# Performance work log

Hardware: AMD Instinct MI355X
Metric: run time of the kernel (lower is better)

## Reference

```python
import jax, jax.numpy as jnp
import numpy as np
from jax import lax

NB, D_MODEL, D_INNER, D_STATE, K, L, BATCH, NCLS, DT_RANK = 3, 512, 1024, 8, 4, 2048, 4, 10, 32


def setup_inputs() -> dict:
    key = jax.random.key(0)
    ks = jax.random.split(key, 12)
    s = 0.02
    inp = {
        "x": jax.random.normal(ks[0], (BATCH, L, D_MODEL), jnp.float32),
        "in_proj_w": s * jax.random.normal(ks[1], (NB, D_MODEL, 2 * D_INNER), jnp.float32),
        "conv_w": s * jax.random.normal(ks[2], (NB, D_INNER, K), jnp.float32),
        "conv_b": jnp.zeros((NB, D_INNER), jnp.float32),
        "x_proj_w": s * jax.random.normal(ks[3], (NB, D_INNER, DT_RANK + 2 * D_STATE), jnp.float32),
        "dt_proj_w": s * jax.random.normal(ks[4], (NB, DT_RANK, D_INNER), jnp.float32),
        "dt_proj_b": jnp.full((NB, D_INNER), -4.0, jnp.float32),
        "A_log": jnp.broadcast_to(jnp.log(jnp.arange(1, D_STATE + 1, dtype=jnp.float32)), (NB, D_INNER, D_STATE)).copy(),
        "D": jnp.ones((NB, D_INNER), jnp.float32),
        "out_proj_w": s * jax.random.normal(ks[5], (NB, D_INNER, D_MODEL), jnp.float32),
        "cls_w": s * jax.random.normal(ks[6], (D_MODEL, NCLS), jnp.float32),
        "cls_b": jnp.zeros((NCLS,), jnp.float32),
    }
    return inp


def _mamba_block(x, Wi, cw, cb, Wx, Wdt, bdt, A_log, Dp, Wo):
    # x: [B, L, d_model]
    Bsz, Lx, _ = x.shape
    d_inner = Dp.shape[0]
    d_state = A_log.shape[-1]
    dt_rank = Wdt.shape[0]
    xz = x @ Wi                               # [B, L, 2*d_inner]
    u, z = jnp.split(xz, 2, axis=-1)
    # causal depthwise conv1d over time
    uc = jnp.swapaxes(u, 1, 2)                # [B, d_inner, L]
    k = cw.shape[-1]
    uc = lax.conv_general_dilated(uc, cw[:, None, :], window_strides=(1,),
                                  padding=[(k - 1, 0)], feature_group_count=d_inner,
                                  dimension_numbers=("NCH", "OIH", "NCH"))
    u = jax.nn.silu(jnp.swapaxes(uc, 1, 2) + cb)   # [B, L, d_inner]
    dbl = u @ Wx                                   # [B, L, dt_rank + 2*d_state]
    dt = dbl[..., :dt_rank]
    Bm = dbl[..., dt_rank:dt_rank + d_state]
    Cm = dbl[..., dt_rank + d_state:]
    delta = jax.nn.softplus(dt @ Wdt + bdt)        # [B, L, d_inner]
    A = -jnp.exp(A_log)                            # [d_inner, d_state]

    def step(h, inp):
        d_t, B_t, C_t, u_t = inp                   # [B,d],[B,n],[B,n],[B,d]
        h = jnp.exp(d_t[..., None] * A) * h + (d_t * u_t)[..., None] * B_t[:, None, :]
        return h, jnp.einsum("bdn,bn->bd", h, C_t)

    xs = (jnp.swapaxes(delta, 0, 1), jnp.swapaxes(Bm, 0, 1),
          jnp.swapaxes(Cm, 0, 1), jnp.swapaxes(u, 0, 1))
    h0 = jnp.zeros((Bsz, d_inner, d_state), x.dtype)
    _, ys = lax.scan(step, h0, xs)                 # ys: [L, B, d_inner]
    y = jnp.swapaxes(ys, 0, 1) + u * Dp
    y = y * jax.nn.silu(z)
    return x + y @ Wo                              # residual


def reference(x, in_proj_w, conv_w, conv_b, x_proj_w, dt_proj_w, dt_proj_b, A_log, D, out_proj_w, cls_w, cls_b):
    nb = in_proj_w.shape[0]
    for i in range(nb):
        x = _mamba_block(x, in_proj_w[i], conv_w[i], conv_b[i], x_proj_w[i],
                         dt_proj_w[i], dt_proj_b[i], A_log[i], D[i], out_proj_w[i])
    pooled = jnp.mean(x, axis=1)                   # AdaptiveAvgPool1d(1) over seq
    return pooled @ cls_w + cls_b                  # [B, num_classes]
```

## Files before the change

kernel.cpp:

```cpp
#include <hip/hip_runtime.h>
#include <cstddef>
#include <cstdint>

#define L_SEQ   2048
#define BATCH_N 4
#define DMODEL  512
#define DINNER  1024
#define DSTATE  8
#define KCONV   4
#define DTRANK  32
#define NBLK    3
#define NCLS_N  10
#define MROWS   (BATCH_N * L_SEQ)
#define DBLW    48
#define NSPLIT  8

#define LC2 16
#define NC2 (L_SEQ / LC2)
#define VD  2
#define SCAN_THREADS 512
#define SCAN_WAVES   (SCAN_THREADS / 64)

#define CGRP 8
#define CPG  (NC2 / CGRP)

typedef __attribute__((ext_vector_type(8))) short bf16x8;
typedef __attribute__((ext_vector_type(4))) short bf16x4;
typedef __attribute__((ext_vector_type(2))) short bf16x2;
typedef __attribute__((ext_vector_type(4))) float f32x4;

__device__ __forceinline__ float sigmoid_fast(float x) { return 1.f / (1.f + __expf(-x)); }
__device__ __forceinline__ float silu_fast(float x)    { return x * sigmoid_fast(x); }
__device__ __forceinline__ float softplus_fast(float x){
    return fmaxf(x, 0.f) + __logf(1.f + __expf(-fabsf(x)));
}
__device__ __forceinline__ float exp2_fast(float x) {
#if __has_builtin(__builtin_amdgcn_exp2f)
    return __builtin_amdgcn_exp2f(x);
#else
    return __expf(x * 0.69314718055994531f);
#endif
}
#define LOG2E 1.44269504088896341f

__device__ __forceinline__ unsigned short f2bf(float f) {
    union { float f; uint32_t u; } v; v.f = f;
    const uint32_t u = v.u;
    return (unsigned short)((u + 0x7fffu + ((u >> 16) & 1u)) >> 16);
}
__device__ __forceinline__ float bf2f(unsigned short h) {
    union { uint32_t u; float f; } v; v.u = ((uint32_t)h) << 16;
    return v.f;
}
__device__ __forceinline__ float bf2f_s(short h) { return bf2f((unsigned short)h); }

__device__ __forceinline__ void load_lds16(const void* g, void* l) {
    __builtin_amdgcn_global_load_lds(
        (const __attribute__((address_space(1))) unsigned int*)g,
        (__attribute__((address_space(3))) unsigned int*)l,
        16, 0, 0);
}

template <int K, int NT, int EPI>
__global__ __launch_bounds__(256) void gemm_bf16(
    const unsigned short* __restrict__ A, int lda,
    const unsigned short* __restrict__ Bt, int ldb,
    int ldc,
    unsigned short* __restrict__ Obf,
    float* __restrict__ pool)
{
    constexpr int BCH   = NT / 8;
    constexpr int NTW   = NT / 32;
    constexpr int STAGE = 8192 + NT * 64;
    constexpr int EPIL  = 128 * (NT + 8);
    constexpr int SMEM  = (STAGE > EPIL) ? STAGE : EPIL;
    __shared__ unsigned short sMem[SMEM];
    unsigned short* sA = sMem;
    unsigned short* sB = sMem + 8192;

    const int tid  = threadIdx.x;
    const int lane = tid & 63;
    const int wave = tid >> 6;
    const int m0 = blockIdx.y * 128;
    const int n0 = blockIdx.x * NT;
    const int wm = (wave >> 1) * 64;
    const int wn = (wave & 1) * (NT / 2);
    const int lm = lane & 15;
    const int lq = lane >> 4;

    const int srow = lane >> 3;
    const int scol = ((lane & 7) ^ srow) * 8;

    f32x4 acc[4][NTW];
    #pragma unroll
    for (int i = 0; i < 4; ++i)
        #pragma unroll
        for (int j = 0; j < NTW; ++j) acc[i][j] = (f32x4){0.f, 0.f, 0.f, 0.f};

    for (int k0 = 0; k0 < K; k0 += 64) {
        #pragma unroll
        for (int c = wave; c < 16; c += 4)
            load_lds16(A + (size_t)(m0 + c * 8 + srow) * lda + k0 + scol, &sA[c * 512]);
        #pragma unroll
        for (int c = wave; c < BCH; c += 4)
            load_lds16(Bt + (size_t)(n0 + c * 8 + srow) * ldb + k0 + scol, &sB[c * 512]);
        __syncthreads();
        #pragma unroll
        for (int ks = 0; ks < 2; ++ks) {
            bf16x8 aF[4], bF[NTW];
            #pragma unroll
            for (int mt = 0; mt < 4; ++mt) {
                const int row = wm + mt * 16 + lm;
                aF[mt] = *(const bf16x8*)&sA[row * 64 + (((ks * 4 + lq) ^ (lm & 7)) * 8)];
            }
            #pragma unroll
            for (int nt = 0; nt < NTW; ++nt) {
                const int row = wn + nt * 16 + lm;
                bF[nt] = *(const bf16x8*)&sB[row * 64 + (((ks * 4 + lq) ^ (lm & 7)) * 8)];
            }
            #pragma unroll
            for (int mt = 0; mt < 4; ++mt)
                #pragma unroll
                for (int nt = 0; nt < NTW; ++nt)
                    acc[mt][nt] = __builtin_amdgcn_mfma_f32_16x16x32_bf16(
                        aF[mt], bF[nt], acc[mt][nt], 0, 0, 0);
        }
        __syncthreads();
    }

    unsigned short* sOut = sMem;
    #pragma unroll
    for (int mt = 0; mt < 4; ++mt) {
        #pragma unroll
        for (int nt = 0; nt < NTW; ++nt) {
            #pragma unroll
            for (int r = 0; r < 4; ++r) {
                const int row = wm + mt * 16 + lq * 4 + r;
                const int col = wn + nt * 16 + lm;
                float v = acc[mt][nt][r];
                if (EPI >= 2) {
                    const size_t gi = (size_t)(m0 + row) * ldc + n0 + col;
                    v += bf2f(Obf[gi]);
                }
                sOut[row * (NT + 8) + col] = f2bf(v);
            }
        }
    }
    __syncthreads();
    #pragma unroll
    for (int j = 0; j < NT / 16; ++j) {
        const int idx = j * 256 + tid;
        const int row = idx / (NT / 8);
        const int cpos = (idx % (NT / 8)) * 8;
        *(bf16x8*)&Obf[(size_t)(m0 + row) * ldc + n0 + cpos] =
            *(const bf16x8*)&sOut[row * (NT + 8) + cpos];
    }
    if (EPI == 3) {
        const int b = m0 >> 11;
        const int col = tid & (NT - 1);
        const int q = tid / NT;
        constexpr int RPQ = 128 / (256 / NT);
        float s = 0.f;
        #pragma unroll
        for (int r = q * RPQ; r < (q + 1) * RPQ; ++r)
            s += bf2f(sOut[r * (NT + 8) + col]);
        atomicAdd(&pool[b * DMODEL + n0 + col], s);
    }
}

__global__ __launch_bounds__(256) void gemm_xproj(
    const unsigned short* __restrict__ ub,
    const unsigned short* __restrict__ Wxt,
    float* __restrict__ Xp)
{
    const int tid = threadIdx.x, lane = tid & 63, wave = tid >> 6;
    const int lm = lane & 15, lq = lane >> 4;
    const int rowA = blockIdx.x * 128 + wave * 32;
    const int split = blockIdx.y;
    const int k0 = split * (DINNER / NSPLIT);

    f32x4 acc[2][3];
    #pragma unroll
    for (int i = 0; i < 2; ++i)
        #pragma unroll
        for (int j = 0; j < 3; ++j) acc[i][j] = (f32x4){0.f, 0.f, 0.f, 0.f};

    #pragma unroll
    for (int kk = 0; kk < DINNER / NSPLIT; kk += 32) {
        const int k = k0 + kk;
        bf16x8 aF[2], bF[3];
        #pragma unroll
        for (int mt = 0; mt < 2; ++mt)
            aF[mt] = *(const bf16x8*)&ub[(size_t)(rowA + mt * 16 + lm) * DINNER + k + lq * 8];
        #pragma unroll
        for (int nt = 0; nt < 3; ++nt)
            bF[nt] = *(const bf16x8*)&Wxt[(size_t)(nt * 16 + lm) * DINNER + k + lq * 8];
        #pragma unroll
        for (int mt = 0; mt < 2; ++mt)
            #pragma unroll
            for (int nt = 0; nt < 3; ++nt)
                acc[mt][nt] = __builtin_amdgcn_mfma_f32_16x16x32_bf16(
                    aF[mt], bF[nt], acc[mt][nt], 0, 0, 0);
    }
    float* dst = Xp + (size_t)split * MROWS * DBLW;
    #pragma unroll
    for (int mt = 0; mt < 2; ++mt)
        #pragma unroll
        for (int nt = 0; nt < 3; ++nt)
            #pragma unroll
            for (int r = 0; r < 4; ++r)
                dst[(size_t)(rowA + mt * 16 + lq * 4 + r) * DBLW
                    + nt * 16 + lm] = acc[mt][nt][r];
}

__global__ __launch_bounds__(256) void transpose_cast(
    const float* __restrict__ in, unsigned short* __restrict__ out,
    int Kdim, int Ndim, size_t in_stride, size_t out_stride)
{
    __shared__ float s[32][33];
    const float* ip = in + blockIdx.z * in_stride;
    unsigned short* op = out + blockIdx.z * out_stride;
    const int bx = blockIdx.x * 32;
    const int by = blockIdx.y * 32;
    const int t = threadIdx.x;
    const int r = t >> 3;
    const int c4 = (t & 7) * 4;

    const int row = by + r;
    if (bx + c4 + 3 < Ndim) {
        float4 v = *(const float4*)&ip[(size_t)row * Ndim + bx + c4];
        s[r][c4 + 0] = v.x; s[r][c4 + 1] = v.y; s[r][c4 + 2] = v.z; s[r][c4 + 3] = v.w;
    } else {
        for (int i = 0; i < 4; ++i) {
            const int col = bx + c4 + i;
            s[r][c4 + i] = (col < Ndim) ? ip[(size_t)row * Ndim + col] : 0.f;
        }
    }
    __syncthreads();
    if (bx + r < Ndim) {
        unsigned short w0 = f2bf(s[c4 + 0][r]), w1 = f2bf(s[c4 + 1][r]);
        unsigned short w2 = f2bf(s[c4 + 2][r]), w3 = f2bf(s[c4 + 3][r]);
        uint2 pk;
        pk.x = (uint32_t)w0 | ((uint32_t)w1 << 16);
        pk.y = (uint32_t)w2 | ((uint32_t)w3 << 16);
        *(uint2*)&op[(size_t)(bx + r) * Kdim + by + c4] = pk;
    }
}

__global__ void cast_init(const float* __restrict__ in, unsigned short* __restrict__ outb,
                          float* __restrict__ pooled_accum, int n4) {
    const int i = blockIdx.x * 256 + threadIdx.x;
    if (i < BATCH_N * DMODEL / 4)
        ((f32x4*)pooled_accum)[i] = (f32x4){0.f, 0.f, 0.f, 0.f};
    if (i >= n4) return;
    float4 v = ((const float4*)in)[i];
    uint2 pk;
    pk.x = (uint32_t)f2bf(v.x) | ((uint32_t)f2bf(v.y) << 16);
    pk.y = (uint32_t)f2bf(v.z) | ((uint32_t)f2bf(v.w) << 16);
    ((uint2*)outb)[i] = pk;
}

__global__ void conv_w_transpose(const float* __restrict__ cw, float* __restrict__ cwt) {
    const int i = blockIdx.x * 256 + threadIdx.x;
    if (i >= NBLK * DINNER * KCONV) return;
    const int blk = i >> 12;
    const int rem = i & 4095;
    const int d = rem >> 2;
    const int k = rem & 3;
    cwt[blk * 4096 + k * DINNER + d] = cw[blk * 4096 + d * KCONV + k];
}

__global__ __launch_bounds__(256) void conv_silu_kernel(
    const unsigned short* __restrict__ xz,
    const float* __restrict__ cwt,
    const float* __restrict__ cb,
    unsigned short* __restrict__ ub)
{
    const int idx = blockIdx.x * 256 + threadIdx.x;
    const int dv = idx & 127;
    const int m  = idx >> 7;
    const int t  = m & (L_SEQ - 1);
    const int d0 = dv * 8;

    float acc[8];
    {
        float4 c0 = *(const float4*)&cb[d0];
        float4 c1 = *(const float4*)&cb[d0 + 4];
        acc[0] = c0.x; acc[1] = c0.y; acc[2] = c0.z; acc[3] = c0.w;
        acc[4] = c1.x; acc[5] = c1.y; acc[6] = c1.z; acc[7] = c1.w;
    }
    #pragma unroll
    for (int k = 0; k < KCONV; ++k) {
        const int tt = t + k - (KCONV - 1);
        if (tt >= 0) {
            bf16x8 xv = *(const bf16x8*)&xz[(size_t)(m - t + tt) * (2 * DINNER) + d0];
            float4 w0 = *(const float4*)&cwt[k * DINNER + d0];
            float4 w1 = *(const float4*)&cwt[k * DINNER + d0 + 4];
            acc[0] = fmaf(bf2f_s(xv[0]), w0.x, acc[0]);
            acc[1] = fmaf(bf2f_s(xv[1]), w0.y, acc[1]);
            acc[2] = fmaf(bf2f_s(xv[2]), w0.z, acc[2]);
            acc[3] = fmaf(bf2f_s(xv[3]), w0.w, acc[3]);
            acc[4] = fmaf(bf2f_s(xv[4]), w1.x, acc[4]);
            acc[5] = fmaf(bf2f_s(xv[5]), w1.y, acc[5]);
            acc[6] = fmaf(bf2f_s(xv[6]), w1.z, acc[6]);
            acc[7] = fmaf(bf2f_s(xv[7]), w1.w, acc[7]);
        }
    }
    bf16x8 o;
    #pragma unroll
    for (int j = 0; j < 8; ++j) o[j] = (short)f2bf(silu_fast(acc[j]));
    *(bf16x8*)&ub[(size_t)m * DINNER + d0] = o;
}

__device__ __forceinline__ void dt_recompute_lds(
    unsigned short* sDelta,
    const float* __restrict__ Xp,
    const unsigned short* __restrict__ Wdtt,
    const float* __restrict__ bdt,
    size_t m0, int lane, int wave)
{
    const int lm = lane & 15, lq = lane >> 4;
    float x[8] = {0.f, 0.f, 0.f, 0.f, 0.f, 0.f, 0.f, 0.f};
    #pragma unroll
    for (int sp = 0; sp < NSPLIT; ++sp) {
        const float* p = &Xp[((size_t)sp * MROWS + m0 + lm) * DBLW + lq * 8];
        float4 x0 = *(const float4*)p;
        float4 x1 = *(const float4*)(p + 4);
        x[0] += x0.x; x[1] += x0.y; x[2] += x0.z; x[3] += x0.w;
        x[4] += x1.x; x[5] += x1.y; x[6] += x1.z; x[7] += x1.w;
    }
    bf16x8 aF;
    #pragma unroll
    for (int j = 0; j < 8; ++j) aF[j] = (short)f2bf(x[j]);

    constexpr int NPW = DINNER / (16 * SCAN_WAVES);
    #pragma unroll
    for (int nt = 0; nt < NPW; ++nt) {
        const int col16 = wave * (DINNER / SCAN_WAVES) + nt * 16;
        bf16x8 bF = *(const bf16x8*)&Wdtt[(size_t)(col16 + lm) * DTRANK + lq * 8];
        f32x4 acc = (f32x4){0.f, 0.f, 0.f, 0.f};
        acc = __builtin_amdgcn_mfma_f32_16x16x32_bf16(aF, bF, acc, 0, 0, 0);
        const float bias = bdt[col16 + lm];
        #pragma unroll
        for (int r = 0; r < 4; ++r)
            sDelta[(lq * 4 + r) * DINNER + col16 + lm] =
                f2bf(softplus_fast(acc[r] + bias));
    }
}

__global__ __launch_bounds__(SCAN_THREADS) void scan_chunk_kernel(
    const unsigned short* __restrict__ ub,
    const float* __restrict__ Xp,
    const unsigned short* __restrict__ Wdtt,
    const float* __restrict__ bdt,
    const float* __restrict__ A_log,
    float* __restrict__ PSbuf)
{
    const int c = blockIdx.x;
    const int b = blockIdx.y;
    const int tid = threadIdx.x;
    const int lane = tid & 63;
    const int wave = tid >> 6;
    const int d0 = tid * VD;

    __shared__ unsigned short sDelta[LC2 * DINNER];
    __shared__ float sB[LC2][DSTATE];

    const size_t m0 = (size_t)b * L_SEQ + c * LC2;

    dt_recompute_lds(sDelta, Xp, Wdtt, bdt, m0, lane, wave);
    if (tid < LC2 * DSTATE) {
        const int r = tid >> 3, n = tid & 7;
        float s = 0.f;
        #pragma unroll
        for (int sp = 0; sp < NSPLIT; ++sp)
            s += Xp[((size_t)sp * MROWS + m0 + r) * DBLW + DTRANK + n];
        sB[r][n] = s;
    }
    __syncthreads();

    float a[DSTATE * VD], S[DSTATE * VD];
    float dtsum[VD];
    #pragma unroll
    for (int v = 0; v < VD; ++v) dtsum[v] = 0.f;
    #pragma unroll
    for (int n = 0; n < DSTATE; ++n)
        #pragma unroll
        for (int v = 0; v < VD; ++v) {
            a[n * VD + v] = -__expf(A_log[(d0 + v) * DSTATE + n]) * LOG2E;
            S[n * VD + v] = 0.f;
        }

    for (int r = 0; r < LC2; ++r) {
        const size_t m = m0 + r;
        bf16x2 dv = *(const bf16x2*)&sDelta[r * DINNER + d0];
        bf16x2 uv = *(const bf16x2*)&ub[m * DINNER + d0];
        float dt[VD], du[VD];
        #pragma unroll
        for (int v = 0; v < VD; ++v) {
            dt[v] = bf2f_s(dv[v]);
            du[v] = dt[v] * bf2f_s(uv[v]);
            dtsum[v] += dt[v];
        }
        #pragma unroll
        for (int n = 0; n < DSTATE; ++n) {
            const float bn = sB[r][n];
            #pragma unroll
            for (int v = 0; v < VD; ++v) {
                const float e = exp2_fast(dt[v] * a[n * VD + v]);
                S[n * VD + v] = fmaf(e, S[n * VD + v], du[v] * bn);
            }
        }
    }

    const size_t nb = (size_t)(b * NC2 + c) * DSTATE;
    #pragma unroll
    for (int n = 0; n < DSTATE; ++n) {
        const float P0 = exp2_fast(a[n * VD + 0] * dtsum[0]);
        const float P1 = exp2_fast(a[n * VD + 1] * dtsum[1]);
        float* dst = &PSbuf[(nb + n) * (DINNER * 2) + (size_t)d0 * 2];
        *(f32x4*)dst = (f32x4){P0, S[n * VD + 0], P1, S[n * VD + 1]};
    }
}

__global__ __launch_bounds__(512) void scan_combine_kernel(
    const float* __restrict__ PSbuf,
    float* __restrict__ Hbuf)
{
    const int dl = threadIdx.x & 63;
    const int g  = threadIdx.x >> 6;
    const int d  = blockIdx.x * 64 + dl;
    const int n  = blockIdx.y;
    const int b  = blockIdx.z;

    __shared__ float sP[CGRP][64];
    __shared__ float sS[CGRP][64];

    const int c0 = g * CPG;
    float Pseg = 1.f, Sseg = 0.f;
    #pragma unroll 4
    for (int cc = 0; cc < CPG; ++cc) {
        const size_t row = (size_t)(b * NC2 + c0 + cc) * DSTATE + n;
        const float2 ps = *(const float2*)&PSbuf[row * (DINNER * 2) + (size_t)d * 2];
        Pseg *= ps.x;
        Sseg = fmaf(ps.x, Sseg, ps.y);
    }
    sP[g][dl] = Pseg;
    sS[g][dl] = Sseg;
    __syncthreads();

    float h = 0.f;
    for (int gg = 0; gg < g; ++gg)
        h = fmaf(sP[gg][dl], h, sS[gg][dl]);

    #pragma unroll 4
    for (int cc = 0; cc < CPG; ++cc) {
        const size_t row = (size_t)(b * NC2 + c0 + cc) * DSTATE + n;
        const float2 ps = *(const float2*)&PSbuf[row * (DINNER * 2) + (size_t)d * 2];
        Hbuf[row * DINNER + d] = h;
        h = fmaf(ps.x, h, ps.y);
    }
}

__global__ __launch_bounds__(SCAN_THREADS) void scan_out_kernel(
    const unsigned short* __restrict__ ub,
    const float* __restrict__ Xp,
    const unsigned short* __restrict__ Wdtt,
    const float* __restrict__ bdt,
    const unsigned short* __restrict__ xz,
    const float* __restrict__ A_log,
    const float* __restrict__ Dp,
    const float* __restrict__ Hin,
    unsigned short* __restrict__ ybuf)
{
    const int c = blockIdx.x;
    const int b = blockIdx.y;
    const int tid = threadIdx.x;
    const int lane = tid & 63;
    const int wave = tid >> 6;
    const int d0 = tid * VD;

    __shared__ unsigned short sDelta[LC2 * DINNER];
    __shared__ float sB[LC2][DSTATE];
    __shared__ float sC[LC2][DSTATE];

    const size_t m0 = (size_t)b * L_SEQ + c * LC2;

    dt_recompute_lds(sDelta, Xp, Wdtt, bdt, m0, lane, wave);
    if (tid < LC2 * 2 * DSTATE) {
        const int r = tid >> 4, j = tid & 15;
        float s = 0.f;
        #pragma unroll
        for (int sp = 0; sp < NSPLIT; ++sp)
            s += Xp[((size_t)sp * MROWS + m0 + r) * DBLW + DTRANK + j];
        if (j < DSTATE) sB[r][j] = s;
        else            sC[r][j - DSTATE] = s;
    }
    __syncthreads();

    float a[DSTATE * VD], h[DSTATE * VD];
    const size_t base = ((size_t)(b * NC2 + c) * DSTATE) * DINNER + d0;
    #pragma unroll
    for (int n = 0; n < DSTATE; ++n) {
        float2 hv = *(const float2*)&Hin[base + (size_t)n * DINNER];
        h[n * VD + 0] = hv.x; h[n * VD + 1] = hv.y;
        #pragma unroll
        for (int v = 0; v < VD; ++v)
            a[n * VD + v] = -__expf(A_log[(d0 + v) * DSTATE + n]) * LOG2E;
    }
    float Dd[VD];
    {
        float2 dv2 = *(const float2*)&Dp[d0];
        Dd[0] = dv2.x; Dd[1] = dv2.y;
    }

    for (int r = 0; r < LC2; ++r) {
        const size_t m = m0 + r;
        bf16x2 dv = *(const bf16x2*)&sDelta[r * DINNER + d0];
        bf16x2 uv = *(const bf16x2*)&ub[m * DINNER + d0];
        bf16x2 zv = *(const bf16x2*)&xz[m * (2 * DINNER) + DINNER + d0];
        float dt[VD], ut[VD], du[VD], acc[VD];
        #pragma unroll
        for (int v = 0; v < VD; ++v) {
            dt[v] = bf2f_s(dv[v]);
            ut[v] = bf2f_s(uv[v]);
            du[v] = dt[v] * ut[v];
            acc[v] = 0.f;
        }
        #pragma unroll
        for (int n = 0; n < DSTATE; ++n) {
            const float bn = sB[r][n];
            const float cn = sC[r][n];
            #pragma unroll
            for (int v = 0; v < VD; ++v) {
                const float e = exp2_fast(dt[v] * a[n * VD + v]);
                h[n * VD + v] = fmaf(e, h[n * VD + v], du[v] * bn);
                acc[v] = fmaf(h[n * VD + v], cn, acc[v]);
            }
        }
        bf16x2 o;
        #pragma unroll
        for (int v = 0; v < VD; ++v)
            o[v] = (short)f2bf(fmaf(ut[v], Dd[v], acc[v]) * silu_fast(bf2f_s(zv[v])));
        *(bf16x2*)&ybuf[m * DINNER + d0] = o;
    }
}

__global__ __launch_bounds__(512) void pool_cls_kernel(
    const float* __restrict__ pooled_accum,
    const float* __restrict__ w,
    const float* __restrict__ bias,
    float* __restrict__ out)
{
    __shared__ float sp[DMODEL];
    const int b = blockIdx.x;
    const int dm = threadIdx.x;
    sp[dm] = pooled_accum[b * DMODEL + dm] * (1.f / (float)L_SEQ);
    __syncthreads();
    if (dm < NCLS_N) {
        float acc = bias[dm];
        for (int k = 0; k < DMODEL; ++k)
            acc = fmaf(sp[k], w[k * NCLS_N + dm], acc);
        out[b * NCLS_N + dm] = acc;
    }
}

extern "C" void kernel_launch(void* const* d_in, const int* in_sizes, int n_in,
                              void* d_out, int out_size, void* d_ws, size_t ws_size,
                              hipStream_t stream) {
    const float* x_in      = (const float*)d_in[0];
    const float* in_proj_w = (const float*)d_in[1];
    const float* conv_w    = (const float*)d_in[2];
    const float* conv_b    = (const float*)d_in[3];
    const float* x_proj_w  = (const float*)d_in[4];
    const float* dt_proj_w = (const float*)d_in[5];
    const float* dt_proj_b = (const float*)d_in[6];
    const float* A_log     = (const float*)d_in[7];
    const float* Dp        = (const float*)d_in[8];
    const float* out_proj_w= (const float*)d_in[9];
    const float* cls_w     = (const float*)d_in[10];
    const float* cls_b     = (const float*)d_in[11];
    float* out = (float*)d_out;

    char* w = (char*)d_ws;
    auto alloc = [&](size_t bytes) { char* p = w; w += (bytes + 255) & ~(size_t)255; return p; };
    unsigned short* xz_bf  = (unsigned short*)alloc((size_t)MROWS * 2 * DINNER * 2);
    unsigned short* ub     = (unsigned short*)alloc((size_t)MROWS * DINNER * 2);
    float*          Xp     = (float*)         alloc((size_t)NSPLIT * MROWS * DBLW * 4);
    float*          PSbuf  = (float*)         alloc((size_t)BATCH_N * NC2 * DSTATE * DINNER * 2 * 4);
    float*          Hbuf   = (float*)         alloc((size_t)BATCH_N * NC2 * DSTATE * DINNER * 4);
    unsigned short* xb     = (unsigned short*)alloc((size_t)MROWS * DMODEL * 2);
    unsigned short* ybuf   = (unsigned short*)alloc((size_t)MROWS * DINNER * 2);
    unsigned short* Wit    = (unsigned short*)alloc((size_t)NBLK * 2048 * 512 * 2);
    unsigned short* Wot    = (unsigned short*)alloc((size_t)NBLK * 512 * 1024 * 2);
    unsigned short* Wxt    = (unsigned short*)alloc((size_t)NBLK * DBLW * 1024 * 2);
    unsigned short* Wdtt   = (unsigned short*)alloc((size_t)NBLK * 1024 * DTRANK * 2);
    float*          cwt    = (float*)         alloc((size_t)NBLK * KCONV * DINNER * 4);
    float*          pooled = (float*)         alloc((size_t)BATCH_N * DMODEL * 4);

    cast_init<<<(MROWS * DMODEL / 4) / 256, 256, 0, stream>>>(
        x_in, xb, pooled, MROWS * DMODEL / 4);
    transpose_cast<<<dim3(2048 / 32, 512 / 32, NBLK), 256, 0, stream>>>(
        in_proj_w, Wit, 512, 2048, (size_t)512 * 2048, (size_t)2048 * 512);
    transpose_cast<<<dim3(512 / 32, 1024 / 32, NBLK), 256, 0, stream>>>(
        out_proj_w, Wot, 1024, 512, (size_t)1024 * 512, (size_t)512 * 1024);
    transpose_cast<<<dim3(2, 1024 / 32, NBLK), 256, 0, stream>>>(
        x_proj_w, Wxt, 1024, DBLW, (size_t)1024 * DBLW, (size_t)DBLW * 1024);
    transpose_cast<<<dim3(1024 / 32, 1, NBLK), 256, 0, stream>>>(
        dt_proj_w, Wdtt, DTRANK, 1024, (size_t)DTRANK * 1024, (size_t)1024 * DTRANK);
    conv_w_transpose<<<(NBLK * DINNER * KCONV + 255) / 256, 256, 0, stream>>>(conv_w, cwt);

    for (int blk = 0; blk < NBLK; ++blk) {
        const unsigned short* Wit_b  = Wit  + (size_t)blk * 2048 * 512;
        const unsigned short* Wot_b  = Wot  + (size_t)blk * 512 * 1024;
        const unsigned short* Wxt_b  = Wxt  + (size_t)blk * DBLW * 1024;
        const unsigned short* Wdtt_b = Wdtt + (size_t)blk * 1024 * DTRANK;
        const float* cwt_b = cwt + (size_t)blk * KCONV * DINNER;
        const float* cb  = conv_b    + (size_t)blk * DINNER;
        const float* bdt = dt_proj_b + (size_t)blk * DINNER;
        const float* Al  = A_log     + (size_t)blk * DINNER * DSTATE;
        const float* Dv  = Dp        + (size_t)blk * DINNER;

        gemm_bf16<512, 128, 0><<<dim3(2048 / 128, MROWS / 128), 256, 0, stream>>>(
            xb, DMODEL, Wit_b, DMODEL, 2 * DINNER, xz_bf, nullptr);
        conv_silu_kernel<<<(MROWS * 128) / 256, 256, 0, stream>>>(
            xz_bf, cwt_b, cb, ub);
        gemm_xproj<<<dim3(MROWS / 128, NSPLIT), 256, 0, stream>>>(ub, Wxt_b, Xp);
        {
            dim3 gridA(NC2, BATCH_N);
            scan_chunk_kernel<<<gridA, SCAN_THREADS, 0, stream>>>(
                ub, Xp, Wdtt_b, bdt, Al, PSbuf);
            scan_combine_kernel<<<dim3(DINNER / 64, DSTATE, BATCH_N), 512, 0, stream>>>(
                PSbuf, Hbuf);
            scan_out_kernel<<<gridA, SCAN_THREADS, 0, stream>>>(
                ub, Xp, Wdtt_b, bdt, xz_bf, Al, Dv, Hbuf, ybuf);
        }
        if (blk < NBLK - 1)
            gemm_bf16<1024, 64, 2><<<dim3(DMODEL / 64, MROWS / 128), 256, 0, stream>>>(
                ybuf, DINNER, Wot_b, DINNER, DMODEL, xb, nullptr);
        else
            gemm_bf16<1024, 64, 3><<<dim3(DMODEL / 64, MROWS / 128), 256, 0, stream>>>(
                ybuf, DINNER, Wot_b, DINNER, DMODEL, xb, pooled);
    }

    pool_cls_kernel<<<BATCH_N, DMODEL, 0, stream>>>(pooled, cls_w, cls_b, out);
}
```

Baseline: 551.1 us.

## Split scan blocks over d_inner halves and pre-reduce x_proj partials

The scan chunk and scan output kernels now handle half of d_inner per block, one channel per thread, which doubles the grid to give more parallelism and lower register pressure. A new xp_reduce kernel sums the split-K x_proj partials once, so the scan kernels no longer each re-read all eight splits. A prep kernel computes -exp(A_log)*log2e once, removing that per-block transcendental work. The cost is an extra launch and buffer, narrower (scalar bf16) global loads, and the dt projection recomputed in twice as many blocks.

```diff
diff --git a/kernel.cpp b/kernel.cpp
--- a/kernel.cpp
+++ b/kernel.cpp
@@ -17,7 +17,7 @@
 
 #define LC2 16
 #define NC2 (L_SEQ / LC2)
-#define VD  2
+#define DHALF (DINNER / 2)
 #define SCAN_THREADS 512
 #define SCAN_WAVES   (SCAN_THREADS / 64)
 
@@ -213,6 +213,23 @@
                     + nt * 16 + lm] = acc[mt][nt][r];
 }
 
+__global__ __launch_bounds__(256) void xp_reduce(
+    const float* __restrict__ Xp, float* __restrict__ dblsum)
+{
+    const int i = blockIdx.x * 256 + threadIdx.x;
+    f32x4 s = (f32x4){0.f, 0.f, 0.f, 0.f};
+    #pragma unroll
+    for (int sp = 0; sp < NSPLIT; ++sp)
+        s += ((const f32x4*)(Xp + (size_t)sp * MROWS * DBLW))[i];
+    ((f32x4*)dblsum)[i] = s;
+}
+
+__global__ void prep_negA(const float* __restrict__ A_log, float* __restrict__ negA) {
+    const int i = blockIdx.x * 256 + threadIdx.x;
+    if (i < NBLK * DINNER * DSTATE)
+        negA[i] = -__expf(A_log[i]) * LOG2E;
+}
+
 __global__ __launch_bounds__(256) void transpose_cast(
     const float* __restrict__ in, unsigned short* __restrict__ out,
     int Kdim, int Ndim, size_t in_stride, size_t out_stride)
@@ -314,112 +331,97 @@
 
 __device__ __forceinline__ void dt_recompute_lds(
     unsigned short* sDelta,
-    const float* __restrict__ Xp,
+    const float* __restrict__ dblsum,
     const unsigned short* __restrict__ Wdtt,
     const float* __restrict__ bdt,
-    size_t m0, int lane, int wave)
+    size_t m0, int lane, int wave, int dbase)
 {
     const int lm = lane & 15, lq = lane >> 4;
-    float x[8] = {0.f, 0.f, 0.f, 0.f, 0.f, 0.f, 0.f, 0.f};
-    #pragma unroll
-    for (int sp = 0; sp < NSPLIT; ++sp) {
-        const float* p = &Xp[((size_t)sp * MROWS + m0 + lm) * DBLW + lq * 8];
+    bf16x8 aF;
+    {
+        const float* p = &dblsum[(m0 + lm) * DBLW + lq * 8];
         float4 x0 = *(const float4*)p;
         float4 x1 = *(const float4*)(p + 4);
-        x[0] += x0.x; x[1] += x0.y; x[2] += x0.z; x[3] += x0.w;
-        x[4] += x1.x; x[5] += x1.y; x[6] += x1.z; x[7] += x1.w;
-    }
-    bf16x8 aF;
-    #pragma unroll
-    for (int j = 0; j < 8; ++j) aF[j] = (short)f2bf(x[j]);
-
-    constexpr int NPW = DINNER / (16 * SCAN_WAVES);
+        aF[0] = (short)f2bf(x0.x); aF[1] = (short)f2bf(x0.y);
+        aF[2] = (short)f2bf(x0.z); aF[3] = (short)f2bf(x0.w);
+        aF[4] = (short)f2bf(x1.x); aF[5] = (short)f2bf(x1.y);
+        aF[6] = (short)f2bf(x1.z); aF[7] = (short)f2bf(x1.w);
+    }
+    constexpr int NPW = DHALF / (16 * SCAN_WAVES);
     #pragma unroll
     for (int nt = 0; nt < NPW; ++nt) {
-        const int col16 = wave * (DINNER / SCAN_WAVES) + nt * 16;
+        const int cloc = wave * (DHALF / SCAN_WAVES) + nt * 16;
+        const int col16 = dbase + cloc;
         bf16x8 bF = *(const bf16x8*)&Wdtt[(size_t)(col16 + lm) * DTRANK + lq * 8];
         f32x4 acc = (f32x4){0.f, 0.f, 0.f, 0.f};
         acc = __builtin_amdgcn_mfma_f32_16x16x32_bf16(aF, bF, acc, 0, 0, 0);
         const float bias = bdt[col16 + lm];
         #pragma unroll
         for (int r = 0; r < 4; ++r)
-            sDelta[(lq * 4 + r) * DINNER + col16 + lm] =
+            sDelta[(lq * 4 + r) * DHALF + cloc + lm] =
                 f2bf(softplus_fast(acc[r] + bias));
     }
 }
 
 __global__ __launch_bounds__(SCAN_THREADS) void scan_chunk_kernel(
     const unsigned short* __restrict__ ub,
-    const float* __restrict__ Xp,
+    const float* __restrict__ dblsum,
     const unsigned short* __restrict__ Wdtt,
     const float* __restrict__ bdt,
-    const float* __restrict__ A_log,
+    const float* __restrict__ negA,
     float* __restrict__ PSbuf)
 {
-    const int c = blockIdx.x;
-    const int b = blockIdx.y;
+    const int c  = blockIdx.x;
+    const int dh = blockIdx.y;
+    const int b  = blockIdx.z;
     const int tid = threadIdx.x;
     const int lane = tid & 63;
     const int wave = tid >> 6;
-    const int d0 = tid * VD;
-
-    __shared__ unsigned short sDelta[LC2 * DINNER];
+    const int dbase = dh * DHALF;
+    const int d = dbase + tid;
+
+    __shared__ unsigned short sDelta[LC2 * DHALF];
     __shared__ float sB[LC2][DSTATE];
 
     const size_t m0 = (size_t)b * L_SEQ + c * LC2;
 
-    dt_recompute_lds(sDelta, Xp, Wdtt, bdt, m0, lane, wave);
+    dt_recompute_lds(sDelta, dblsum, Wdtt, bdt, m0, lane, wave, dbase);
     if (tid < LC2 * DSTATE) {
         const int r = tid >> 3, n = tid & 7;
-        float s = 0.f;
-        #pragma unroll
-        for (int sp = 0; sp < NSPLIT; ++sp)
-            s += Xp[((size_t)sp * MROWS + m0 + r) * DBLW + DTRANK + n];
-        sB[r][n] = s;
+        sB[r][n] = dblsum[(m0 + r) * DBLW + DTRANK + n];
     }
     __syncthreads();
 
-    float a[DSTATE * VD], S[DSTATE * VD];
-    float dtsum[VD];
-    #pragma unroll
-    for (int v = 0; v < VD; ++v) dtsum[v] = 0.f;
-    #pragma unroll
-    for (int n = 0; n < DSTATE; ++n)
-        #pragma unroll
-        for (int v = 0; v < VD; ++v) {
-            a[n * VD + v] = -__expf(A_log[(d0 + v) * DSTATE + n]) * LOG2E;
-            S[n * VD + v] = 0.f;
-        }
+    float a[DSTATE], S[DSTATE];
+    {
+        float4 a0 = *(const float4*)&negA[(size_t)d * DSTATE];
+        float4 a1 = *(const float4*)&negA[(size_t)d * DSTATE + 4];
+        a[0] = a0.x; a[1] = a0.y; a[2] = a0.z; a[3] = a0.w;
+        a[4] = a1.x; a[5] = a1.y; a[6] = a1.z; a[7] = a1.w;
+    }
+    #pragma unroll
+    for (int n = 0; n < DSTATE; ++n) S[n] = 0.f;
+    float dtsum = 0.f;
 
     for (int r = 0; r < LC2; ++r) {
         const size_t m = m0 + r;
-        bf16x2 dv = *(const bf16x2*)&sDelta[r * DINNER + d0];
-        bf16x2 uv = *(const bf16x2*)&ub[m * DINNER + d0];
-        float dt[VD], du[VD];
-        #pragma unroll
-        for (int v = 0; v < VD; ++v) {
-            dt[v] = bf2f_s(dv[v]);
-            du[v] = dt[v] * bf2f_s(uv[v]);
-            dtsum[v] += dt[v];
+        const float dt = bf2f(sDelta[r * DHALF + tid]);
+        const float du = dt * bf2f(ub[m * DINNER + d]);
+        dtsum += dt;
+        #pragma unroll
+        for (int n = 0; n < DSTATE; ++n) {
+            const float e = exp2_fast(dt * a[n]);
+            S[n] = fmaf(e, S[n], du * sB[r][n]);
         }
-        #pragma unroll
-        for (int n = 0; n < DSTATE; ++n) {
-            const float bn = sB[r][n];
-            #pragma unroll
-            for (int v = 0; v < VD; ++v) {
-                const float e = exp2_fast(dt[v] * a[n * VD + v]);
-                S[n * VD + v] = fmaf(e, S[n * VD + v], du[v] * bn);
-            }
-        }
     }
 
     const size_t nb = (size_t)(b * NC2 + c) * DSTATE;
     #pragma unroll
     for (int n = 0; n < DSTATE; ++n) {
-        const float P0 = exp2_fast(a[n * VD + 0] * dtsum[0]);
-        const float P1 = exp2_fast(a[n * VD + 1] * dtsum[1]);
-        float* dst = &PSbuf[(nb + n) * (DINNER * 2) + (size_t)d0 * 2];
-        *(f32x4*)dst = (f32x4){P0, S[n * VD + 0], P1, S[n * VD + 1]};
+        float2 ps;
+        ps.x = exp2_fast(a[n] * dtsum);
+        ps.y = S[n];
+        *(float2*)&PSbuf[(nb + n) * (DINNER * 2) + (size_t)d * 2] = ps;
     }
 }
 
@@ -464,85 +466,66 @@
 
 __global__ __launch_bounds__(SCAN_THREADS) void scan_out_kernel(
     const unsigned short* __restrict__ ub,
-    const float* __restrict__ Xp,
+    const float* __restrict__ dblsum,
     const unsigned short* __restrict__ Wdtt,
     const float* __restrict__ bdt,
     const unsigned short* __restrict__ xz,
-    const float* __restrict__ A_log,
+    const float* __restrict__ negA,
     const float* __restrict__ Dp,
     const float* __restrict__ Hin,
     unsigned short* __restrict__ ybuf)
 {
-    const int c = blockIdx.x;
-    const int b = blockIdx.y;
+    const int c  = blockIdx.x;
+    const int dh = blockIdx.y;
+    const int b  = blockIdx.z;
     const int tid = threadIdx.x;
     const int lane = tid & 63;
     const int wave = tid >> 6;
-    const int d0 = tid * VD;
-
-    __shared__ unsigned short sDelta[LC2 * DINNER];
+    const int dbase = dh * DHALF;
+    const int d = dbase + tid;
+
+    __shared__ unsigned short sDelta[LC2 * DHALF];
     __shared__ float sB[LC2][DSTATE];
     __shared__ float sC[LC2][DSTATE];
 
     const size_t m0 = (size_t)b * L_SEQ + c * LC2;
 
-    dt_recompute_lds(sDelta, Xp, Wdtt, bdt, m0, lane, wave);
+    dt_recompute_lds(sDelta, dblsum, Wdtt, bdt, m0, lane, wave, dbase);
     if (tid < LC2 * 2 * DSTATE) {
         const int r = tid >> 4, j = tid & 15;
-        float s = 0.f;
-        #pragma unroll
-        for (int sp = 0; sp < NSPLIT; ++sp)
-            s += Xp[((size_t)sp * MROWS + m0 + r) * DBLW + DTRANK + j];
-        if (j < DSTATE) sB[r][j] = s;
-        else            sC[r][j - DSTATE] = s;
+        const float v = dblsum[(m0 + r) * DBLW + DTRANK + j];
+        if (j < DSTATE) sB[r][j] = v;
+        else            sC[r][j - DSTATE] = v;
     }
     __syncthreads();
 
-    float a[DSTATE * VD], h[DSTATE * VD];
-    const size_t base = ((size_t)(b * NC2 + c) * DSTATE) * DINNER + d0;
-    #pragma unroll
-    for (int n = 0; n < DSTATE; ++n) {
-        float2 hv = *(const float2*)&Hin[base + (size_t)n * DINNER];
-        h[n * VD + 0] = hv.x; h[n * VD + 1] = hv.y;
-        #pragma unroll
-        for (int v = 0; v < VD; ++v)
-            a[n * VD + v] = -__expf(A_log[(d0 + v) * DSTATE + n]) * LOG2E;
-    }
-    float Dd[VD];
+    float a[DSTATE], h[DSTATE];
     {
-        float2 dv2 = *(const float2*)&Dp[d0];
-        Dd[0] = dv2.x; Dd[1] = dv2.y;
-    }
+        float4 a0 = *(const float4*)&negA[(size_t)d * DSTATE];
+        float4 a1 = *(const float4*)&negA[(size_t)d * DSTATE + 4];
+        a[0] = a0.x; a[1] = a0.y; a[2] = a0.z; a[3] = a0.w;
+        a[4] = a1.x; a[5] = a1.y; a[6] = a1.z; a[7] = a1.w;
+    }
+    const size_t base = ((size_t)(b * NC2 + c) * DSTATE) * DINNER + d;
+    #pragma unroll
+    for (int n = 0; n < DSTATE; ++n)
+        h[n] = Hin[base + (size_t)n * DINNER];
+    const float Dd = Dp[d];
 
     for (int r = 0; r < LC2; ++r) {
         const size_t m = m0 + r;
-        bf16x2 dv = *(const bf16x2*)&sDelta[r * DINNER + d0];
-        bf16x2 uv = *(const bf16x2*)&ub[m * DINNER + d0];
-        bf16x2 zv = *(const bf16x2*)&xz[m * (2 * DINNER) + DINNER + d0];
-        float dt[VD], ut[VD], du[VD], acc[VD];
-        #pragma unroll
-        for (int v = 0; v < VD; ++v) {
-            dt[v] = bf2f_s(dv[v]);
-            ut[v] = bf2f_s(uv[v]);
-            du[v] = dt[v] * ut[v];
-            acc[v] = 0.f;
+        const float dt = bf2f(sDelta[r * DHALF + tid]);
+        const float ut = bf2f(ub[m * DINNER + d]);
+        const float zt = bf2f(xz[m * (2 * DINNER) + DINNER + d]);
+        const float du = dt * ut;
+        float acc = 0.f;
+        #pragma unroll
+        for (int n = 0; n < DSTATE; ++n) {
+            const float e = exp2_fast(dt * a[n]);
+            h[n] = fmaf(e, h[n], du * sB[r][n]);
+            acc = fmaf(h[n], sC[r][n], acc);
         }
-        #pragma unroll
-        for (int n = 0; n < DSTATE; ++n) {
-            const float bn = sB[r][n];
-            const float cn = sC[r][n];
-            #pragma unroll
-            for (int v = 0; v < VD; ++v) {
-                const float e = exp2_fast(dt[v] * a[n * VD + v]);
-                h[n * VD + v] = fmaf(e, h[n * VD + v], du[v] * bn);
-                acc[v] = fmaf(h[n * VD + v], cn, acc[v]);
-            }
-        }
-        bf16x2 o;
-        #pragma unroll
-        for (int v = 0; v < VD; ++v)
-            o[v] = (short)f2bf(fmaf(ut[v], Dd[v], acc[v]) * silu_fast(bf2f_s(zv[v])));
-        *(bf16x2*)&ybuf[m * DINNER + d0] = o;
+        ybuf[m * DINNER + d] = f2bf(fmaf(ut, Dd, acc) * silu_fast(zt));
     }
 }
 
@@ -587,6 +570,7 @@
     unsigned short* xz_bf  = (unsigned short*)alloc((size_t)MROWS * 2 * DINNER * 2);
     unsigned short* ub     = (unsigned short*)alloc((size_t)MROWS * DINNER * 2);
     float*          Xp     = (float*)         alloc((size_t)NSPLIT * MROWS * DBLW * 4);
+    float*          dblsum = (float*)         alloc((size_t)MROWS * DBLW * 4);
     float*          PSbuf  = (float*)         alloc((size_t)BATCH_N * NC2 * DSTATE * DINNER * 2 * 4);
     float*          Hbuf   = (float*)         alloc((size_t)BATCH_N * NC2 * DSTATE * DINNER * 4);
     unsigned short* xb     = (unsigned short*)alloc((size_t)MROWS * DMODEL * 2);
@@ -596,6 +580,7 @@
     unsigned short* Wxt    = (unsigned short*)alloc((size_t)NBLK * DBLW * 1024 * 2);
     unsigned short* Wdtt   = (unsigned short*)alloc((size_t)NBLK * 1024 * DTRANK * 2);
     float*          cwt    = (float*)         alloc((size_t)NBLK * KCONV * DINNER * 4);
+    float*          negA   = (float*)         alloc((size_t)NBLK * DINNER * DSTATE * 4);
     float*          pooled = (float*)         alloc((size_t)BATCH_N * DMODEL * 4);
 
     cast_init<<<(MROWS * DMODEL / 4) / 256, 256, 0, stream>>>(
@@ -609,6 +594,7 @@
     transpose_cast<<<dim3(1024 / 32, 1, NBLK), 256, 0, stream>>>(
         dt_proj_w, Wdtt, DTRANK, 1024, (size_t)DTRANK * 1024, (size_t)1024 * DTRANK);
     conv_w_transpose<<<(NBLK * DINNER * KCONV + 255) / 256, 256, 0, stream>>>(conv_w, cwt);
+    prep_negA<<<(NBLK * DINNER * DSTATE + 255) / 256, 256, 0, stream>>>(A_log, negA);
 
     for (int blk = 0; blk < NBLK; ++blk) {
         const unsigned short* Wit_b  = Wit  + (size_t)blk * 2048 * 512;
@@ -618,7 +604,7 @@
         const float* cwt_b = cwt + (size_t)blk * KCONV * DINNER;
         const float* cb  = conv_b    + (size_t)blk * DINNER;
         const float* bdt = dt_proj_b + (size_t)blk * DINNER;
-        const float* Al  = A_log     + (size_t)blk * DINNER * DSTATE;
+        const float* nA  = negA      + (size_t)blk * DINNER * DSTATE;
         const float* Dv  = Dp        + (size_t)blk * DINNER;
 
         gemm_bf16<512, 128, 0><<<dim3(2048 / 128, MROWS / 128), 256, 0, stream>>>(
@@ -626,14 +612,15 @@
         conv_silu_kernel<<<(MROWS * 128) / 256, 256, 0, stream>>>(
             xz_bf, cwt_b, cb, ub);
         gemm_xproj<<<dim3(MROWS / 128, NSPLIT), 256, 0, stream>>>(ub, Wxt_b, Xp);
+        xp_reduce<<<(MROWS * DBLW / 4) / 256, 256, 0, stream>>>(Xp, dblsum);
         {
-            dim3 gridA(NC2, BATCH_N);
+            dim3 gridA(NC2, 2, BATCH_N);
             scan_chunk_kernel<<<gridA, SCAN_THREADS, 0, stream>>>(
-                ub, Xp, Wdtt_b, bdt, Al, PSbuf);
+                ub, dblsum, Wdtt_b, bdt, nA, PSbuf);
             scan_combine_kernel<<<dim3(DINNER / 64, DSTATE, BATCH_N), 512, 0, stream>>>(
                 PSbuf, Hbuf);
             scan_out_kernel<<<gridA, SCAN_THREADS, 0, stream>>>(
-                ub, Xp, Wdtt_b, bdt, xz_bf, Al, Dv, Hbuf, ybuf);
+                ub, dblsum, Wdtt_b, bdt, xz_bf, nA, Dv, Hbuf, ybuf);
         }
         if (blk < NBLK - 1)
             gemm_bf16<1024, 64, 2><<<dim3(DMODEL / 64, MROWS / 128), 256, 0, stream>>>(
```

Measured after the change: 521.5 us. -5.4%, faster.
